# Optimization experiments

Hardware: AMD Instinct MI355X
Metric: run time of the kernel (lower is better)

The kernel has to match this reference:

```python
import jax, jax.numpy as jnp
import numpy as np

NUM_HEADS = 12
EPS = 1e-6


def setup_inputs() -> dict:
    key = jax.random.key(0)
    k1, k2, k3, k4, k5 = jax.random.split(key, 5)
    B, N, C = 8, 4096, 768
    scale = 1.0 / np.sqrt(C)
    return {
        "x": jax.random.normal(k1, (B, N, C), dtype=jnp.float32),
        "W_qkv": jax.random.normal(k2, (C, 3 * C), dtype=jnp.float32) * scale,
        "b_qkv": jax.random.normal(k3, (3 * C,), dtype=jnp.float32) * 0.02,
        "W_proj": jax.random.normal(k4, (C, C), dtype=jnp.float32) * scale,
        "b_proj": jax.random.normal(k5, (C,), dtype=jnp.float32) * 0.02,
    }


def reference(x, W_qkv, b_qkv, W_proj, b_proj):
    B, N, C = x.shape
    H = NUM_HEADS
    D = C // H
    # qkv projection -> (3, B, H, N, D)
    qkv = (x @ W_qkv + b_qkv).reshape(B, N, 3, H, D).transpose(2, 0, 3, 1, 4)
    q, k, v = qkv[0], qkv[1], qkv[2]
    q = jax.nn.sigmoid(q)
    k = jax.nn.sigmoid(k)
    ksum = k.sum(axis=2)  # [B,H,D]
    qsum = q.sum(axis=2)  # [B,H,D]
    # incoming/outgoing flow normalizers, [B,H,N]
    sink_incoming = 1.0 / (jnp.einsum('bhnd,bhd->bhn', q + EPS, ksum + EPS) + EPS)
    source_outgoing = 1.0 / (jnp.einsum('bhnd,bhd->bhn', k + EPS, qsum + EPS) + EPS)
    conserved_sink = jnp.einsum(
        'bhnd,bhd->bhn', q + EPS, (k * source_outgoing[..., None]).sum(axis=2) + EPS) + EPS
    conserved_source = jnp.einsum(
        'bhnd,bhd->bhn', k + EPS, (q * sink_incoming[..., None]).sum(axis=2) + EPS) + EPS
    conserved_source = jnp.clip(conserved_source, -1.0, 1.0)
    sink_allocation = jax.nn.sigmoid(conserved_sink * (float(N) / float(N)))
    source_competition = jax.nn.softmax(conserved_source, axis=-1) * float(N)
    # linear attention: kv = k^T @ (v * competition), [B,H,D,D]
    kv = jnp.einsum('bhnd,bhne->bhde', k, v * source_competition[..., None])
    x_update = jnp.einsum('bhnd,bhde->bhne', q, kv)
    x_update = x_update * sink_incoming[..., None] * sink_allocation[..., None]
    out = x_update.transpose(0, 2, 1, 3).reshape(B, N, C)
    out = out @ W_proj + b_proj
    return jax.nn.sigmoid(2.0 * out)
```

## Files before the change

kernel.cpp:

```cpp
#include <hip/hip_runtime.h>
#include <stdint.h>

#define EPSF 1e-6f

typedef unsigned short u16;
typedef __attribute__((ext_vector_type(8))) short short8;
typedef __attribute__((ext_vector_type(4))) float f32x4;

__device__ __forceinline__ float us2f(u16 u) {
  union { float f; unsigned int i; } c; c.i = ((unsigned int)u) << 16; return c.f;
}
__device__ __forceinline__ u16 f2bfu(float f) {
  union { float f; unsigned int i; } c; c.f = f;
  unsigned int i = c.i;
  return (u16)((i + 0x7FFFu + ((i >> 16) & 1u)) >> 16);
}
__device__ __forceinline__ float sigm(float x) { return 1.f / (1.f + __expf(-x)); }

typedef __attribute__((address_space(3))) unsigned int lds_u32;
typedef const __attribute__((address_space(1))) unsigned int glb_u32;
__device__ __forceinline__ void gl_lds16(const u16* g, u16* l) {
  __builtin_amdgcn_global_load_lds((glb_u32*)g, (lds_u32*)l, 16, 0, 0);
}

__global__ void k_cvt_x(const float* __restrict__ in, u16* __restrict__ out) {
  const int i = blockIdx.x * 256 + threadIdx.x;
  float4 v = ((const float4*)in)[i];
  ushort4 o;
  o.x = f2bfu(v.x); o.y = f2bfu(v.y); o.z = f2bfu(v.z); o.w = f2bfu(v.w);
  ((ushort4*)out)[i] = o;
}

__global__ void k_transpose(const float* __restrict__ in, u16* __restrict__ out, int R, int C) {
  __shared__ float tile[32][33];
  const int tx = threadIdx.x & 31, ty = threadIdx.x >> 5;
  const int c0 = blockIdx.x << 5, r0 = blockIdx.y << 5;
  for (int i = ty; i < 32; i += 8) tile[i][tx] = in[(size_t)(r0 + i) * C + c0 + tx];
  __syncthreads();
  for (int i = ty; i < 32; i += 8) out[(size_t)(c0 + i) * R + r0 + tx] = f2bfu(tile[tx][i]);
}

template <int MODE>
__global__ __launch_bounds__(256) void k_gemm(
    const u16* __restrict__ A, const u16* __restrict__ BT,
    const float* __restrict__ bias,
    u16* __restrict__ qkvo, float* __restrict__ qsum, float* __restrict__ ksum,
    float* __restrict__ outf)
{
  __shared__ __align__(16) u16 sA[2][128 * 32];
  __shared__ __align__(16) u16 sB[2][128 * 32];
  const int tid = threadIdx.x;
  const int lane = tid & 63;
  const int wid = tid >> 6;
  const int wr = wid >> 1, wc = wid & 1;
  const int nx = gridDim.x;
  int lid = blockIdx.y * nx + blockIdx.x;
  const int q8 = (nx * gridDim.y) >> 3;
  lid = (lid & 7) * q8 + (lid >> 3);
  const int m0 = (lid / nx) << 7;
  const int n0 = (lid % nx) << 7;
  const int srow = lane >> 2;
  const int cgsw = ((lane & 3) ^ ((lane >> 3) & 3)) << 3;

  const u16* ga0 = A  + (size_t)(m0 + (wid << 4) + srow) * 768 + cgsw;
  const u16* ga1 = A  + (size_t)(m0 + ((wid + 4) << 4) + srow) * 768 + cgsw;
  const u16* gb0 = BT + (size_t)(n0 + (wid << 4) + srow) * 768 + cgsw;
  const u16* gb1 = BT + (size_t)(n0 + ((wid + 4) << 4) + srow) * 768 + cgsw;

  f32x4 acc[4][4];
#pragma unroll
  for (int i = 0; i < 4; ++i)
#pragma unroll
    for (int j = 0; j < 4; ++j) acc[i][j] = (f32x4){0.f, 0.f, 0.f, 0.f};

#define STAGE(buf, ktel)                                        \
  do {                                                          \
    gl_lds16(ga0 + (ktel), &sA[buf][(wid) * 512]);              \
    gl_lds16(ga1 + (ktel), &sA[buf][(wid + 4) * 512]);          \
    gl_lds16(gb0 + (ktel), &sB[buf][(wid) * 512]);              \
    gl_lds16(gb1 + (ktel), &sB[buf][(wid + 4) * 512]);          \
  } while (0)

  STAGE(0, 0);
  asm volatile("s_waitcnt vmcnt(0)" ::: "memory");
  __syncthreads();

  const int r16 = lane & 15;
  const int ksw = (((lane >> 4) ^ ((r16 >> 1) & 3)) << 3);
  int cur = 0;
  for (int kt = 1; kt <= 24; ++kt) {
    if (kt < 24) {
      if (cur) STAGE(0, kt * 32); else STAGE(1, kt * 32);
    }
    const u16* pa = &sA[cur][0];
    const u16* pb = &sB[cur][0];
    short8 af[4], bfv[4];
#pragma unroll
    for (int i = 0; i < 4; ++i)
      af[i] = *(const short8*)(pa + ((wr << 6) + (i << 4) + r16) * 32 + ksw);
#pragma unroll
    for (int j = 0; j < 4; ++j)
      bfv[j] = *(const short8*)(pb + ((wc << 6) + (j << 4) + r16) * 32 + ksw);
#pragma unroll
    for (int i = 0; i < 4; ++i)
#pragma unroll
      for (int j = 0; j < 4; ++j)
        acc[i][j] = __builtin_amdgcn_mfma_f32_16x16x32_bf16(af[i], bfv[j], acc[i][j], 0, 0, 0);
    asm volatile("s_waitcnt vmcnt(0)" ::: "memory");
    __syncthreads();
    cur ^= 1;
  }
#undef STAGE

  if (MODE == 0) {
    const int colc = n0 + (wc << 6);
    const bool sg = (colc < 1536);
    float jsum[4] = {0.f, 0.f, 0.f, 0.f};
#pragma unroll
    for (int i = 0; i < 4; ++i) {
      const int rowb = m0 + (wr << 6) + (i << 4) + ((lane >> 4) << 2);
#pragma unroll
      for (int j = 0; j < 4; ++j) {
        const int col = colc + (j << 4) + r16;
        const float bcol = bias[col];
        if (sg) {
#pragma unroll
          for (int rg = 0; rg < 4; ++rg) {
            const float val = sigm(acc[i][j][rg] + bcol);
            jsum[j] += val;
            qkvo[(size_t)(rowb + rg) * 2304 + col] = f2bfu(val);
          }
        } else {
#pragma unroll
          for (int rg = 0; rg < 4; ++rg)
            qkvo[(size_t)(rowb + rg) * 2304 + col] = f2bfu(acc[i][j][rg] + bcol);
        }
      }
    }
    if (sg) {
#pragma unroll
      for (int j = 0; j < 4; ++j) {
        jsum[j] += __shfl_xor(jsum[j], 16, 64);
        jsum[j] += __shfl_xor(jsum[j], 32, 64);
      }
      if (lane < 16) {
        const int b12 = (m0 >> 12) * 12;
        float* sdst = (colc >= 768) ? ksum : qsum;
        const int cb = (colc >= 768) ? colc - 768 : colc;
#pragma unroll
        for (int j = 0; j < 4; ++j)
          atomicAdd(&sdst[(b12 << 6) + cb + (j << 4) + r16], jsum[j]);
      }
    }
  } else {
#pragma unroll
    for (int i = 0; i < 4; ++i) {
      const int rowb = m0 + (wr << 6) + (i << 4) + ((lane >> 4) << 2);
#pragma unroll
      for (int j = 0; j < 4; ++j) {
        const int col = n0 + (wc << 6) + (j << 4) + r16;
        const float bcol = bias[col];
#pragma unroll
        for (int rg = 0; rg < 4; ++rg)
          outf[(size_t)(rowb + rg) * 768 + col] = sigm(2.f * (acc[i][j][rg] + bcol));
      }
    }
  }
}

__global__ __launch_bounds__(256) void k_flow1(
    const u16* __restrict__ qkv,
    const float* __restrict__ qsum, const float* __restrict__ ksum,
    float* __restrict__ si_out, float* __restrict__ qsi, float* __restrict__ kso)
{
  const int bh = blockIdx.x >> 3, sp = blockIdx.x & 7;
  const int lane = threadIdx.x & 63, wid = threadIdx.x >> 6;
  const int j = lane & 15;
  const int grp = (wid << 2) | (lane >> 4);
  const u16* base = qkv + (size_t)(bh / 12) * 4096 * 2304 + (bh % 12) * 64;
  float ke[4], qe[4];
#pragma unroll
  for (int t = 0; t < 4; ++t) {
    ke[t] = ksum[(bh << 6) + (j << 2) + t] + EPSF;
    qe[t] = qsum[(bh << 6) + (j << 2) + t] + EPSF;
  }
  float Sk = ke[0] + ke[1] + ke[2] + ke[3];
  float Sq = qe[0] + qe[1] + qe[2] + qe[3];
#pragma unroll
  for (int msk = 1; msk < 16; msk <<= 1) { Sk += __shfl_xor(Sk, msk, 64); Sq += __shfl_xor(Sq, msk, 64); }
  const float cK = EPSF * Sk + EPSF;
  const float cQ = EPSF * Sq + EPSF;
  float aq0 = 0, aq1 = 0, aq2 = 0, aq3 = 0, ak0 = 0, ak1 = 0, ak2 = 0, ak3 = 0;
  const int nbase = sp << 9;
  for (int it = 0; it < 32; ++it) {
    const int n = nbase + (it << 4) + grp;
    const size_t ro = (size_t)n * 2304 + (j << 2);
    const uint64_t lq = *(const uint64_t*)(base + ro);
    const uint64_t lk = *(const uint64_t*)(base + ro + 768);
    const float q0 = us2f((u16)lq), q1 = us2f((u16)(lq >> 16)), q2 = us2f((u16)(lq >> 32)), q3 = us2f((u16)(lq >> 48));
    const float k0 = us2f((u16)lk), k1 = us2f((u16)(lk >> 16)), k2 = us2f((u16)(lk >> 32)), k3 = us2f((u16)(lk >> 48));
    float dq = q0 * ke[0] + q1 * ke[1] + q2 * ke[2] + q3 * ke[3];
    float dk = k0 * qe[0] + k1 * qe[1] + k2 * qe[2] + k3 * qe[3];
#pragma unroll
    for (int msk = 1; msk < 16; msk <<= 1) { dq += __shfl_xor(dq, msk, 64); dk += __shfl_xor(dk, msk, 64); }
    const float si = 1.f / (dq + cK);
    const float so = 1.f / (dk + cQ);
    if (j == 0) si_out[(bh << 12) + n] = si;
    aq0 += q0 * si; aq1 += q1 * si; aq2 += q2 * si; aq3 += q3 * si;
    ak0 += k0 * so; ak1 += k1 * so; ak2 += k2 * so; ak3 += k3 * so;
  }
  __shared__ float redq[16][64];
  __shared__ float redk[16][64];
  redq[grp][(j << 2) + 0] = aq0; redq[grp][(j << 2) + 1] = aq1;
  redq[grp][(j << 2) + 2] = aq2; redq[grp][(j << 2) + 3] = aq3;
  redk[grp][(j << 2) + 0] = ak0; redk[grp][(j << 2) + 1] = ak1;
  redk[grp][(j << 2) + 2] = ak2; redk[grp][(j << 2) + 3] = ak3;
  __syncthreads();
  if (threadIdx.x < 64) {
    float s1 = 0.f, s2 = 0.f;
#pragma unroll
    for (int g = 0; g < 16; ++g) { s1 += redq[g][threadIdx.x]; s2 += redk[g][threadIdx.x]; }
    atomicAdd(&qsi[(bh << 6) + threadIdx.x], s1);
    atomicAdd(&kso[(bh << 6) + threadIdx.x], s2);
  }
}

__global__ __launch_bounds__(256) void k_fkv(
    const u16* __restrict__ qkv,
    const float* __restrict__ qsi, const float* __restrict__ kso,
    const float* __restrict__ si_in,
    float* __restrict__ mo, float* __restrict__ sumexp, float* __restrict__ kvm)
{
  __shared__ __align__(16) u16 smem[2 * 64 * 136];
  u16* kT = smem;
  u16* vT = smem + 64 * 136;
  const int tid = threadIdx.x;
  const int bh = blockIdx.x >> 3, sp = blockIdx.x & 7;
  const int lane = tid & 63, wid = tid >> 6;
  const int r16 = lane & 15, g = lane >> 4;
  const u16* base = qkv + (size_t)(bh / 12) * 4096 * 2304 + (bh % 12) * 64;
  const float* sib = si_in + ((size_t)bh << 12);
  float* mob = mo + ((size_t)bh << 12);

  const int d0 = (tid & 7) << 3;
  float qie[8], soe[8];
#pragma unroll
  for (int u = 0; u < 8; ++u) {
    qie[u] = qsi[(bh << 6) + d0 + u] + EPSF;
    soe[u] = kso[(bh << 6) + d0 + u] + EPSF;
  }
  float Sq = qsi[(bh << 6) + lane] + EPSF;
  float Sk = kso[(bh << 6) + lane] + EPSF;
#pragma unroll
  for (int m = 1; m < 64; m <<= 1) { Sq += __shfl_xor(Sq, m, 64); Sk += __shfl_xor(Sk, m, 64); }
  const float cR = EPSF * Sq + EPSF;
  const float cS = EPSF * Sk + EPSF;

  f32x4 acc[4][4];
#pragma unroll
  for (int i = 0; i < 4; ++i)
#pragma unroll
    for (int j = 0; j < 4; ++j) acc[i][j] = (f32x4){0.f, 0.f, 0.f, 0.f};

  const int nf = (wid << 5) + (g << 3);
  float esum = 0.f;

  for (int st = 0; st < 4; ++st) {
    const int nst = (sp << 9) + (st << 7);
#pragma unroll
    for (int i = 0; i < 4; ++i) {
      const int c = tid + (i << 8);
      const int nl = c >> 3;
      const int ng = nst + nl;
      const u16* rp = base + (size_t)ng * 2304 + d0;
      short8 q8 = *(const short8*)(rp);
      short8 k8 = *(const short8*)(rp + 768);
      short8 v8 = *(const short8*)(rp + 1536);
      float pcs = 0.f, pcr = 0.f;
#pragma unroll
      for (int u = 0; u < 8; ++u) {
        pcs += us2f((u16)q8[u]) * soe[u];
        pcr += us2f((u16)k8[u]) * qie[u];
      }
#pragma unroll
      for (int m = 1; m < 8; m <<= 1) { pcs += __shfl_xor(pcs, m, 64); pcr += __shfl_xor(pcr, m, 64); }
      float cr = pcr + cR;
      cr = fminf(1.f, fmaxf(-1.f, cr));
      const float ev = __expf(cr);
      const int col = nl ^ (d0 & 56);
#pragma unroll
      for (int u = 0; u < 8; ++u) {
        kT[(d0 + u) * 136 + col] = f2bfu(us2f((u16)k8[u]) * ev);
        vT[(d0 + u) * 136 + col] = (u16)(unsigned short)v8[u];
      }
      if ((tid & 7) == 0) {
        mob[ng] = sib[ng] * sigm(pcs + cS);
        esum += ev;
      }
    }
    __syncthreads();

    short8 af[4], bf[4];
#pragma unroll
    for (int mi = 0; mi < 4; ++mi) {
      const int row = (mi << 4) + r16;
      af[mi] = *(const short8*)&kT[row * 136 + (nf ^ (row & 56))];
    }
#pragma unroll
    for (int nj = 0; nj < 4; ++nj) {
      const int row = (nj << 4) + r16;
      bf[nj] = *(const short8*)&vT[row * 136 + (nf ^ (row & 56))];
    }
#pragma unroll
    for (int mi = 0; mi < 4; ++mi)
#pragma unroll
      for (int nj = 0; nj < 4; ++nj)
        acc[mi][nj] = __builtin_amdgcn_mfma_f32_16x16x32_bf16(af[mi], bf[nj], acc[mi][nj], 0, 0, 0);
    __syncthreads();
  }

  float* red = (float*)smem;
  float* kvb = kvm + ((size_t)bh << 12);
#pragma unroll
  for (int half = 0; half < 2; ++half) {
#pragma unroll
    for (int m2 = 0; m2 < 2; ++m2) {
      const int mi = (half << 1) + m2;
#pragma unroll
      for (int nj = 0; nj < 4; ++nj)
#pragma unroll
        for (int rg = 0; rg < 4; ++rg)
          red[(wid << 11) + (((m2 << 4) + (g << 2) + rg) << 6) + (nj << 4) + r16] = acc[mi][nj][rg];
    }
    __syncthreads();
    const int base2 = tid << 3;
#pragma unroll
    for (int u2 = 0; u2 < 2; ++u2) {
      const int o = base2 + (u2 << 2);
      float4 s0 = *(const float4*)&red[o];
      float4 s1 = *(const float4*)&red[2048 + o];
      float4 s2 = *(const float4*)&red[4096 + o];
      float4 s3 = *(const float4*)&red[6144 + o];
      s0.x += s1.x + s2.x + s3.x;
      s0.y += s1.y + s2.y + s3.y;
      s0.z += s1.z + s2.z + s3.z;
      s0.w += s1.w + s2.w + s3.w;
      const int gi = (half << 11) + o;
      atomicAdd(&kvb[gi + 0], s0.x);
      atomicAdd(&kvb[gi + 1], s0.y);
      atomicAdd(&kvb[gi + 2], s0.z);
      atomicAdd(&kvb[gi + 3], s0.w);
    }
    __syncthreads();
  }

  esum += __shfl_xor(esum, 8, 64);
  esum += __shfl_xor(esum, 16, 64);
  esum += __shfl_xor(esum, 32, 64);
  if (lane == 0) atomicAdd(&sumexp[bh], esum);
}

__global__ __launch_bounds__(256) void k_xup(
    const u16* __restrict__ qkv, const float* __restrict__ kvm,
    const float* __restrict__ m_arr, const float* __restrict__ sumexp,
    u16* __restrict__ attn)
{
  const int bh = blockIdx.y;
  const int n0 = blockIdx.x << 7;
  const int b = bh / 12, h = bh % 12;
  __shared__ __align__(16) u16 qs[128 * 72];
  __shared__ __align__(16) u16 kvs[64 * 72];
  const int tid = threadIdx.x, lane = tid & 63, wid = tid >> 6;
  const u16* qg = qkv + (size_t)b * 4096 * 2304 + (size_t)n0 * 2304 + h * 64;
#pragma unroll
  for (int i = 0; i < 4; ++i) {
    const int c = tid + (i << 8);
    const int nl = c >> 3, d0 = (c & 7) << 3;
    *(short8*)&qs[nl * 72 + d0] = *(const short8*)(qg + (size_t)nl * 2304 + d0);
  }
  const float* kvg = kvm + ((size_t)bh << 12);
#pragma unroll
  for (int i = 0; i < 4; ++i) {
    const int idx = (tid << 2) + (i << 10);
    const int d = idx >> 6, e0 = idx & 63;
    float4 vv = *(const float4*)(kvg + idx);
    kvs[(e0 + 0) * 72 + d] = f2bfu(vv.x);
    kvs[(e0 + 1) * 72 + d] = f2bfu(vv.y);
    kvs[(e0 + 2) * 72 + d] = f2bfu(vv.z);
    kvs[(e0 + 3) * 72 + d] = f2bfu(vv.w);
  }
  __syncthreads();
  const float scale = 4096.f / sumexp[bh];
  const int r16 = lane & 15, kg8 = (lane >> 4) << 3;
  f32x4 acc[2][4];
#pragma unroll
  for (int i = 0; i < 2; ++i)
#pragma unroll
    for (int j = 0; j < 4; ++j) acc[i][j] = (f32x4){0.f, 0.f, 0.f, 0.f};
#pragma unroll
  for (int kk = 0; kk < 2; ++kk) {
    short8 af[2], bfv[4];
#pragma unroll
    for (int mi = 0; mi < 2; ++mi)
      af[mi] = *(const short8*)&qs[((wid << 5) + (mi << 4) + r16) * 72 + (kk << 5) + kg8];
#pragma unroll
    for (int nj = 0; nj < 4; ++nj)
      bfv[nj] = *(const short8*)&kvs[((nj << 4) + r16) * 72 + (kk << 5) + kg8];
#pragma unroll
    for (int mi = 0; mi < 2; ++mi)
#pragma unroll
      for (int nj = 0; nj < 4; ++nj)
        acc[mi][nj] = __builtin_amdgcn_mfma_f32_16x16x32_bf16(af[mi], bfv[nj], acc[mi][nj], 0, 0, 0);
  }
#pragma unroll
  for (int mi = 0; mi < 2; ++mi) {
#pragma unroll
    for (int rg = 0; rg < 4; ++rg) {
      const int n = n0 + (wid << 5) + (mi << 4) + ((lane >> 4) << 2) + rg;
      const float mult = m_arr[((size_t)bh << 12) + n] * scale;
#pragma unroll
      for (int nj = 0; nj < 4; ++nj) {
        const int e = (nj << 4) + r16;
        attn[((size_t)(b * 4096 + n)) * 768 + (h << 6) + e] = f2bfu(acc[mi][nj][rg] * mult);
      }
    }
  }
}

extern "C" void kernel_launch(void* const* d_in, const int* in_sizes, int n_in,
                              void* d_out, int out_size, void* d_ws, size_t ws_size,
                              hipStream_t stream)
{
  (void)in_sizes; (void)n_in; (void)out_size; (void)ws_size;
  const float* x     = (const float*)d_in[0];
  const float* Wqkv  = (const float*)d_in[1];
  const float* bqkv  = (const float*)d_in[2];
  const float* Wproj = (const float*)d_in[3];
  const float* bproj = (const float*)d_in[4];
  float* out = (float*)d_out;

  char* ws = (char*)d_ws;
  size_t off = 0;
  auto alloc = [&](size_t bytes) -> char* {
    char* p = ws + off;
    off += (bytes + 255) & ~(size_t)255;
    return p;
  };
  u16* qkv  = (u16*)alloc(150994944);
  u16* xbf  = (u16*)alloc(50331648);
  u16* WqT  = (u16*)alloc(3538944);
  u16* WpT  = (u16*)alloc(1179648);
  float* si = (float*)alloc(1572864);
  float* mb = (float*)alloc(1572864);
  char* zbase = ws + off;
  float* qsum   = (float*)alloc(24576);
  float* ksum   = (float*)alloc(24576);
  float* qsi    = (float*)alloc(24576);
  float* kso    = (float*)alloc(24576);
  float* sumexp = (float*)alloc(512);
  float* kvm    = (float*)alloc(1572864);
  const size_t zbytes = (size_t)((ws + off) - zbase);

  hipMemsetAsync(zbase, 0, zbytes, stream);
  k_cvt_x<<<24576, 256, 0, stream>>>(x, xbf);
  k_transpose<<<dim3(72, 24), 256, 0, stream>>>(Wqkv, WqT, 768, 2304);
  k_transpose<<<dim3(24, 24), 256, 0, stream>>>(Wproj, WpT, 768, 768);
  k_gemm<0><<<dim3(18, 256), 256, 0, stream>>>(xbf, WqT, bqkv, qkv, qsum, ksum, nullptr);
  k_flow1<<<768, 256, 0, stream>>>(qkv, qsum, ksum, si, qsi, kso);
  k_fkv<<<768, 256, 0, stream>>>(qkv, qsi, kso, si, mb, sumexp, kvm);
  k_xup<<<dim3(32, 96), 256, 0, stream>>>(qkv, kvm, mb, sumexp, xbf);
  k_gemm<1><<<dim3(6, 256), 256, 0, stream>>>(xbf, WpT, bproj, nullptr, nullptr, nullptr, out);
}
```

Before: 443.4 us.

## Enlarge GEMM tiles to 256x256 with 4-stage LDS pipeline and 8 waves

Reworks the bf16 MFMA GEMM used for the QKV and output projections. Tiles grow from 128x128 to 256x256, each block runs 512 threads (8 waves, each owning 128x64), and the LDS double buffer becomes a 4-deep ring with three stages prefetched. Each iteration waits with a partial vmcnt instead of draining all loads, and raises wave priority around the MFMA section. This aims to improve data reuse per tile and hide global-to-LDS latency, at the cost of 128KB LDS per block and more accumulator registers, which lowers occupancy and grid size.

```diff
diff --git a/kernel.cpp b/kernel.cpp
--- a/kernel.cpp
+++ b/kernel.cpp
@@ -41,128 +41,137 @@
 }
 
 template <int MODE>
-__global__ __launch_bounds__(256) void k_gemm(
+__global__ __launch_bounds__(512, 2) void k_gemm(
     const u16* __restrict__ A, const u16* __restrict__ BT,
     const float* __restrict__ bias,
     u16* __restrict__ qkvo, float* __restrict__ qsum, float* __restrict__ ksum,
     float* __restrict__ outf)
 {
-  __shared__ __align__(16) u16 sA[2][128 * 32];
-  __shared__ __align__(16) u16 sB[2][128 * 32];
+  __shared__ __align__(16) u16 smem[65536];
   const int tid = threadIdx.x;
   const int lane = tid & 63;
   const int wid = tid >> 6;
-  const int wr = wid >> 1, wc = wid & 1;
+  const int wm = wid >> 2, wn = wid & 3;
   const int nx = gridDim.x;
   int lid = blockIdx.y * nx + blockIdx.x;
   const int q8 = (nx * gridDim.y) >> 3;
   lid = (lid & 7) * q8 + (lid >> 3);
-  const int m0 = (lid / nx) << 7;
-  const int n0 = (lid % nx) << 7;
-  const int srow = lane >> 2;
-  const int cgsw = ((lane & 3) ^ ((lane >> 3) & 3)) << 3;
-
-  const u16* ga0 = A  + (size_t)(m0 + (wid << 4) + srow) * 768 + cgsw;
-  const u16* ga1 = A  + (size_t)(m0 + ((wid + 4) << 4) + srow) * 768 + cgsw;
-  const u16* gb0 = BT + (size_t)(n0 + (wid << 4) + srow) * 768 + cgsw;
-  const u16* gb1 = BT + (size_t)(n0 + ((wid + 4) << 4) + srow) * 768 + cgsw;
-
-  f32x4 acc[4][4];
-#pragma unroll
-  for (int i = 0; i < 4; ++i)
+  const int m0 = (lid / nx) << 8;
+  const int n0 = (lid % nx) << 8;
+
+  const int rowS = tid >> 2;
+  const int sub  = tid & 3;
+  const int subx = sub ^ ((rowS >> 1) & 3);
+  const u16* gA = A  + (size_t)(m0 + rowS) * 768 + (subx << 3);
+  const u16* gB = BT + (size_t)(n0 + rowS) * 768 + (subx << 3);
+  const int dstc = tid << 3;
+
+  const int r16 = lane & 15;
+  const int sgrp = lane >> 4;
+  int offA[8], offB[4];
+#pragma unroll
+  for (int mi = 0; mi < 8; ++mi) {
+    const int ra = (wm << 7) + (mi << 4) + r16;
+    offA[mi] = ra * 32 + ((sgrp ^ ((ra >> 1) & 3)) << 3);
+  }
+#pragma unroll
+  for (int nj = 0; nj < 4; ++nj) {
+    const int rb = (wn << 6) + (nj << 4) + r16;
+    offB[nj] = rb * 32 + ((sgrp ^ ((rb >> 1) & 3)) << 3);
+  }
+
+  f32x4 acc[8][4];
+#pragma unroll
+  for (int i = 0; i < 8; ++i)
 #pragma unroll
     for (int j = 0; j < 4; ++j) acc[i][j] = (f32x4){0.f, 0.f, 0.f, 0.f};
 
-#define STAGE(buf, ktel)                                        \
-  do {                                                          \
-    gl_lds16(ga0 + (ktel), &sA[buf][(wid) * 512]);              \
-    gl_lds16(ga1 + (ktel), &sA[buf][(wid + 4) * 512]);          \
-    gl_lds16(gb0 + (ktel), &sB[buf][(wid) * 512]);              \
-    gl_lds16(gb1 + (ktel), &sB[buf][(wid + 4) * 512]);          \
+#define STAGE(kh)                                                   \
+  do {                                                              \
+    const int khs = ((kh) > 23 ? 23 : (kh)) << 5;                   \
+    const int so = ((kh) & 3) << 13;                                \
+    gl_lds16(gA + khs,         &smem[so + dstc]);                   \
+    gl_lds16(gA + 98304 + khs, &smem[so + dstc + 4096]);            \
+    gl_lds16(gB + khs,         &smem[32768 + so + dstc]);           \
+    gl_lds16(gB + 98304 + khs, &smem[32768 + so + dstc + 4096]);    \
   } while (0)
 
-  STAGE(0, 0);
+  STAGE(0); STAGE(1); STAGE(2);
+
+  for (int kh = 0; kh < 24; ++kh) {
+    asm volatile("s_waitcnt vmcnt(8)" ::: "memory");
+    __builtin_amdgcn_s_barrier();
+    __builtin_amdgcn_sched_barrier(0);
+    STAGE(kh + 3);
+    const u16* pa = &smem[(kh & 3) << 13];
+    const u16* pb = pa + 32768;
+    short8 bf[4];
+#pragma unroll
+    for (int nj = 0; nj < 4; ++nj) bf[nj] = *(const short8*)(pb + offB[nj]);
+    __builtin_amdgcn_s_setprio(1);
+#pragma unroll
+    for (int mi = 0; mi < 8; ++mi) {
+      const short8 av = *(const short8*)(pa + offA[mi]);
+#pragma unroll
+      for (int nj = 0; nj < 4; ++nj)
+        acc[mi][nj] = __builtin_amdgcn_mfma_f32_16x16x32_bf16(av, bf[nj], acc[mi][nj], 0, 0, 0);
+    }
+    __builtin_amdgcn_s_setprio(0);
+  }
+#undef STAGE
   asm volatile("s_waitcnt vmcnt(0)" ::: "memory");
-  __syncthreads();
-
-  const int r16 = lane & 15;
-  const int ksw = (((lane >> 4) ^ ((r16 >> 1) & 3)) << 3);
-  int cur = 0;
-  for (int kt = 1; kt <= 24; ++kt) {
-    if (kt < 24) {
-      if (cur) STAGE(0, kt * 32); else STAGE(1, kt * 32);
-    }
-    const u16* pa = &sA[cur][0];
-    const u16* pb = &sB[cur][0];
-    short8 af[4], bfv[4];
-#pragma unroll
-    for (int i = 0; i < 4; ++i)
-      af[i] = *(const short8*)(pa + ((wr << 6) + (i << 4) + r16) * 32 + ksw);
-#pragma unroll
-    for (int j = 0; j < 4; ++j)
-      bfv[j] = *(const short8*)(pb + ((wc << 6) + (j << 4) + r16) * 32 + ksw);
-#pragma unroll
-    for (int i = 0; i < 4; ++i)
-#pragma unroll
-      for (int j = 0; j < 4; ++j)
-        acc[i][j] = __builtin_amdgcn_mfma_f32_16x16x32_bf16(af[i], bfv[j], acc[i][j], 0, 0, 0);
-    asm volatile("s_waitcnt vmcnt(0)" ::: "memory");
-    __syncthreads();
-    cur ^= 1;
-  }
-#undef STAGE
 
   if (MODE == 0) {
-    const int colc = n0 + (wc << 6);
+    const int colc = n0 + (wn << 6);
     const bool sg = (colc < 1536);
     float jsum[4] = {0.f, 0.f, 0.f, 0.f};
 #pragma unroll
-    for (int i = 0; i < 4; ++i) {
-      const int rowb = m0 + (wr << 6) + (i << 4) + ((lane >> 4) << 2);
-#pragma unroll
-      for (int j = 0; j < 4; ++j) {
-        const int col = colc + (j << 4) + r16;
+    for (int mi = 0; mi < 8; ++mi) {
+      const int rowb = m0 + (wm << 7) + (mi << 4) + ((lane >> 4) << 2);
+#pragma unroll
+      for (int nj = 0; nj < 4; ++nj) {
+        const int col = colc + (nj << 4) + r16;
         const float bcol = bias[col];
         if (sg) {
 #pragma unroll
           for (int rg = 0; rg < 4; ++rg) {
-            const float val = sigm(acc[i][j][rg] + bcol);
-            jsum[j] += val;
+            const float val = sigm(acc[mi][nj][rg] + bcol);
+            jsum[nj] += val;
             qkvo[(size_t)(rowb + rg) * 2304 + col] = f2bfu(val);
           }
         } else {
 #pragma unroll
           for (int rg = 0; rg < 4; ++rg)
-            qkvo[(size_t)(rowb + rg) * 2304 + col] = f2bfu(acc[i][j][rg] + bcol);
+            qkvo[(size_t)(rowb + rg) * 2304 + col] = f2bfu(acc[mi][nj][rg] + bcol);
         }
       }
     }
     if (sg) {
 #pragma unroll
-      for (int j = 0; j < 4; ++j) {
-        jsum[j] += __shfl_xor(jsum[j], 16, 64);
-        jsum[j] += __shfl_xor(jsum[j], 32, 64);
+      for (int nj = 0; nj < 4; ++nj) {
+        jsum[nj] += __shfl_xor(jsum[nj], 16, 64);
+        jsum[nj] += __shfl_xor(jsum[nj], 32, 64);
       }
       if (lane < 16) {
         const int b12 = (m0 >> 12) * 12;
         float* sdst = (colc >= 768) ? ksum : qsum;
         const int cb = (colc >= 768) ? colc - 768 : colc;
 #pragma unroll
-        for (int j = 0; j < 4; ++j)
-          atomicAdd(&sdst[(b12 << 6) + cb + (j << 4) + r16], jsum[j]);
+        for (int nj = 0; nj < 4; ++nj)
+          atomicAdd(&sdst[(b12 << 6) + cb + (nj << 4) + r16], jsum[nj]);
       }
     }
   } else {
 #pragma unroll
-    for (int i = 0; i < 4; ++i) {
-      const int rowb = m0 + (wr << 6) + (i << 4) + ((lane >> 4) << 2);
-#pragma unroll
-      for (int j = 0; j < 4; ++j) {
-        const int col = n0 + (wc << 6) + (j << 4) + r16;
+    for (int mi = 0; mi < 8; ++mi) {
+      const int rowb = m0 + (wm << 7) + (mi << 4) + ((lane >> 4) << 2);
+#pragma unroll
+      for (int nj = 0; nj < 4; ++nj) {
+        const int col = n0 + (wn << 6) + (nj << 4) + r16;
         const float bcol = bias[col];
 #pragma unroll
         for (int rg = 0; rg < 4; ++rg)
-          outf[(size_t)(rowb + rg) * 768 + col] = sigm(2.f * (acc[i][j][rg] + bcol));
+          outf[(size_t)(rowb + rg) * 768 + col] = sigm(2.f * (acc[mi][nj][rg] + bcol));
       }
     }
   }
@@ -465,9 +474,9 @@
   k_cvt_x<<<24576, 256, 0, stream>>>(x, xbf);
   k_transpose<<<dim3(72, 24), 256, 0, stream>>>(Wqkv, WqT, 768, 2304);
   k_transpose<<<dim3(24, 24), 256, 0, stream>>>(Wproj, WpT, 768, 768);
-  k_gemm<0><<<dim3(18, 256), 256, 0, stream>>>(xbf, WqT, bqkv, qkv, qsum, ksum, nullptr);
+  k_gemm<0><<<dim3(9, 128), 512, 0, stream>>>(xbf, WqT, bqkv, qkv, qsum, ksum, nullptr);
   k_flow1<<<768, 256, 0, stream>>>(qkv, qsum, ksum, si, qsi, kso);
   k_fkv<<<768, 256, 0, stream>>>(qkv, qsi, kso, si, mb, sumexp, kvm);
   k_xup<<<dim3(32, 96), 256, 0, stream>>>(qkv, kvm, mb, sumexp, xbf);
-  k_gemm<1><<<dim3(6, 256), 256, 0, stream>>>(xbf, WpT, bproj, nullptr, nullptr, nullptr, out);
-}
+  k_gemm<1><<<dim3(3, 128), 512, 0, stream>>>(xbf, WpT, bproj, nullptr, nullptr, nullptr, out);
+}
```

New measurement: 416.8 us. -6.0%, faster.
